# Kernel tuning notes

Measured on AMD Instinct MI355X. Metric: run time of the kernel, lower is better.

Reference implementation:

```python
import jax, jax.numpy as jnp
import numpy as np

RADIUS = 5
ALPHA = 200.0
N, H, W = 8, 352, 352


def _maxpool5(x):
    # F.max_pool2d(kernel=5, stride=1, padding=2); torch pads with -inf for max pool
    return jax.lax.reduce_window(
        x, -jnp.inf, jax.lax.max,
        window_dimensions=(1, 1, 5, 5), window_strides=(1, 1, 1, 1),
        padding=[(0, 0), (0, 0), (2, 2), (2, 2)])


def setup_inputs() -> dict:
    key = jax.random.key(0)
    k1, k2 = jax.random.split(key)
    pred = jax.random.uniform(k1, (N, 1, H, W), dtype=jnp.float32)
    feat = jax.random.uniform(k2, (N, 3, H, W), dtype=jnp.float32)
    return {"pred": pred, "feat": feat}


def reference(pred, feat):
    # interpolate(pred, scale_factor=1.0) and interpolate(feat, size=pred HxW)
    # are identities here (same spatial size, bilinear align_corners).
    sal_map = pred
    image_ = feat

    # contour mask: dilation - erosion of thresholded saliency
    lbl = (sal_map > 0.5).astype(sal_map.dtype)
    ero = 1.0 - _maxpool5(1.0 - lbl)
    dil = _maxpool5(lbl)
    mask = dil - ero  # (N,1,H,W)

    features = jnp.concatenate([image_, sal_map], axis=1)  # (N,4,H,W)
    n, c, h, w = features.shape
    r = RADIUS
    # zero padding matches F.unfold's implicit zero padding
    fpad = jnp.pad(features, ((0, 0), (0, 0), (r, r), (r, r)))
    center_rgb = features[:, :3]   # (N,3,H,W)
    center_sal = features[:, 3:]   # (N,1,H,W)

    # On-the-fly sliding-window reduction instead of materializing the
    # (N,4,11,11,H,W) unfold tensor. 121 static shifts (fixed small set).
    loss_map = jnp.zeros((n, 1, h, w), dtype=features.dtype)
    for dy in range(2 * r + 1):
        for dx in range(2 * r + 1):
            win = fpad[:, :, dy:dy + h, dx:dx + w]  # (N,4,H,W)
            d_rgb = win[:, :3] - center_rgb
            d_sal = jnp.abs(win[:, 3:] - center_sal)
            wgt = jnp.exp(-ALPHA * jnp.sum(d_rgb * d_rgb, axis=1, keepdims=True))
            loss_map = loss_map + wgt * d_sal

    loss = jnp.sum(loss_map * mask) / (jnp.sum(mask) + 1e-6)
    return loss
```

## Files before the change

kernel.cpp:

```cpp
#include <hip/hip_runtime.h>

#define NB 8
#define HH 352
#define WW 352
#define TX 32
#define TY 32
#define TLH 37
#define TLW 42
#define LSTRIDE 43
#define MH 37
#define MW 42
#define MSTRIDE 44
#define TILES_X 11
#define TILES_Y 11
#define NBLK (TILES_X * TILES_Y * NB)

#define RGB_SCALE 16.98644781888824f

typedef float f32x2 __attribute__((ext_vector_type(2)));

__device__ __forceinline__ float elem(float4 q, int c) {
    return c == 0 ? q.x : c == 1 ? q.y : c == 2 ? q.z : q.w;
}

__device__ __forceinline__ void tap_pair(const float4& w, float mq,
                                         f32x2 ncx, f32x2 ncy, f32x2 ncz, f32x2 ncw,
                                         f32x2& accP, f32x2& accQ) {
    f32x2 d0 = ncx + w.x;
    f32x2 d1 = ncy + w.y;
    f32x2 d2 = ncz + w.z;
    f32x2 s  = d0 * d0;
    s += d1 * d1;
    s += d2 * d2;
    f32x2 ds = ncw + w.w;
    f32x2 v;
    v.x = __builtin_amdgcn_exp2f(-s.x) * fabsf(ds.x);
    v.y = __builtin_amdgcn_exp2f(-s.y) * fabsf(ds.y);
    accP += v;
    f32x2 mqv; mqv.x = mq; mqv.y = mq;
    accQ += v * mqv;
}

__device__ __forceinline__ void tap_scalar(const float4& w, float mq,
                                           float ncx, float ncy, float ncz, float ncw,
                                           float& aP, float& aQ) {
    float d0 = w.x + ncx, d1 = w.y + ncy, d2 = w.z + ncz;
    float s = fmaf(d0, d0, fmaf(d1, d1, d2 * d2));
    float v = __builtin_amdgcn_exp2f(-s) * fabsf(w.w + ncw);
    aP += v;
    aQ = fmaf(v, mq, aQ);
}

__global__ __launch_bounds__(256, 2)
void btm_loss_kernel(const float* __restrict__ pred,
                     const float* __restrict__ feat,
                     float2* __restrict__ partials) {
    __shared__ __align__(16) float4 tile[TLH * LSTRIDE];
    __shared__ __align__(16) float  maskp[MH * MSTRIDE];
    __shared__ unsigned long long hbuf[41];
    __shared__ unsigned long long nhbuf[41];
    __shared__ unsigned long long Mbuf[37];
    __shared__ float2 wred[4];

    const int bid = blockIdx.x;
    const int tx_blk = bid % TILES_X;
    const int ty_blk = (bid / TILES_X) % TILES_Y;
    const int n = bid / (TILES_X * TILES_Y);
    const int x0 = tx_blk * TX;
    const int y0 = ty_blk * TY;

    const size_t plane = (size_t)HH * WW;
    const float* fr = feat + ((size_t)n * 3 + 0) * plane;
    const float* fg = feat + ((size_t)n * 3 + 1) * plane;
    const float* fb = feat + ((size_t)n * 3 + 2) * plane;
    const float* ps = pred + (size_t)n * plane;

    const int t = threadIdx.x;

    {
        const int wv = t >> 6, ln = t & 63;
        for (int r = wv; r < 41; r += 4) {
            int gy = y0 + r - 2;
            int gx = x0 - 7 + ln;
            bool inimg = ((unsigned)gy < (unsigned)HH) &&
                         ((unsigned)gx < (unsigned)WW) && (ln < 46);
            float sv = inimg ? ps[gy * WW + gx] : 0.f;
            unsigned long long lb = __ballot(inimg && (sv > 0.5f));
            unsigned long long nb = __ballot(inimg && (sv <= 0.5f));
            unsigned long long a2 = lb | (lb >> 1); a2 |= (a2 >> 2); a2 |= (lb >> 4);
            unsigned long long b2 = nb | (nb >> 1); b2 |= (b2 >> 2); b2 |= (nb >> 4);
            if (ln == 0) { hbuf[r] = a2; nhbuf[r] = b2; }
        }
    }

    for (int i = t; i < TLH * TLW; i += 256) {
        int lr = i / TLW;
        int lc = i - lr * TLW;
        int gy = y0 + lr;
        int gx = x0 + lc - 5;
        float4 v = make_float4(0.f, 0.f, 0.f, 0.f);
        if ((unsigned)gy < (unsigned)HH && (unsigned)gx < (unsigned)WW) {
            int gi = gy * WW + gx;
            v.x = fr[gi] * RGB_SCALE;
            v.y = fg[gi] * RGB_SCALE;
            v.z = fb[gi] * RGB_SCALE;
            v.w = ps[gi];
        }
        tile[lr * LSTRIDE + lc] = v;
    }
    __syncthreads();

    if (t < 37) {
        int lo = 5 - x0; if (lo < 0) lo = 0;
        int hi = WW + 5 - x0; if (hi > 42) hi = 42;
        unsigned long long cm = ((1ull << hi) - 1) & ~((1ull << lo) - 1);
        unsigned long long D = hbuf[t], E = nhbuf[t];
        #pragma unroll
        for (int k = 1; k < 5; ++k) { D |= hbuf[t + k]; E |= nhbuf[t + k]; }
        Mbuf[t] = (y0 + t < HH) ? (D & E & cm) : 0ull;
    }
    __syncthreads();

    for (int i = t; i < MH * MW; i += 256) {
        int mr = i / MW, mc = i - mr * MW;
        maskp[mr * MSTRIDE + mc] = (float)((Mbuf[mr] >> mc) & 1ull);
    }
    __syncthreads();

    const int txq = t & 7;
    const int ty  = t >> 3;
    const int px0 = txq * 4;

    const float4* trow = tile + ty * LSTRIDE + px0;
    const float*  mrow = maskp + ty * MSTRIDE + px0;

    float4 c0 = trow[5], c1 = trow[6], c2 = trow[7], c3 = trow[8];
    f32x2 n01x = {-c0.x, -c1.x}, n01y = {-c0.y, -c1.y}, n01z = {-c0.z, -c1.z}, n01w = {-c0.w, -c1.w};
    f32x2 n23x = {-c2.x, -c3.x}, n23y = {-c2.y, -c3.y}, n23z = {-c2.z, -c3.z}, n23w = {-c2.w, -c3.w};

    f32x2 aP01 = {0.f, 0.f}, aP23 = {0.f, 0.f};
    f32x2 aQ01 = {0.f, 0.f}, aQ23 = {0.f, 0.f};
    float sP0 = 0.f, sP1 = 0.f, sP2 = 0.f, sP3 = 0.f, sQ = 0.f;

    float4 mf0[3];
    #pragma unroll
    for (int q = 0; q < 3; ++q) mf0[q] = *(const float4*)&mrow[4 + 4 * q];
    {
        float4 w0[8];
        #pragma unroll
        for (int j = 0; j < 8; ++j) w0[j] = trow[6 + j];

        tap_scalar(w0[0], elem(mf0[0], 2), n01x.x, n01y.x, n01z.x, n01w.x, sP0, sQ);
        #pragma unroll
        for (int j = 1; j <= 4; ++j)
            tap_pair(w0[j], elem(mf0[(j + 2) >> 2], (j + 2) & 3), n01x, n01y, n01z, n01w, aP01, aQ01);
        tap_scalar(w0[5], elem(mf0[1], 3), n01x.y, n01y.y, n01z.y, n01w.y, sP1, sQ);
        tap_scalar(w0[2], elem(mf0[1], 0), n23x.x, n23y.x, n23z.x, n23w.x, sP2, sQ);
        #pragma unroll
        for (int j = 3; j <= 6; ++j)
            tap_pair(w0[j], elem(mf0[(j + 2) >> 2], (j + 2) & 3), n23x, n23y, n23z, n23w, aP23, aQ23);
        tap_scalar(w0[7], elem(mf0[2], 1), n23x.y, n23y.y, n23z.y, n23w.y, sP3, sQ);
    }

    #pragma unroll 1
    for (int dy = 1; dy <= 5; ++dy) {
        float4 w[14];
        #pragma unroll
        for (int j = 0; j < 14; ++j) w[j] = trow[dy * LSTRIDE + j];
        float4 mf[4];
        const float* mro = mrow + dy * MSTRIDE;
        #pragma unroll
        for (int q = 0; q < 4; ++q) mf[q] = *(const float4*)&mro[4 * q];

        tap_scalar(w[0], elem(mf[0], 0), n01x.x, n01y.x, n01z.x, n01w.x, sP0, sQ);
        #pragma unroll
        for (int j = 1; j <= 10; ++j)
            tap_pair(w[j], elem(mf[j >> 2], j & 3), n01x, n01y, n01z, n01w, aP01, aQ01);
        tap_scalar(w[11], elem(mf[2], 3), n01x.y, n01y.y, n01z.y, n01w.y, sP1, sQ);
        tap_scalar(w[2],  elem(mf[0], 2), n23x.x, n23y.x, n23z.x, n23w.x, sP2, sQ);
        #pragma unroll
        for (int j = 3; j <= 12; ++j)
            tap_pair(w[j], elem(mf[j >> 2], j & 3), n23x, n23y, n23z, n23w, aP23, aQ23);
        tap_scalar(w[13], elem(mf[3], 1), n23x.y, n23y.y, n23z.y, n23w.y, sP3, sQ);
    }

    float m0 = mf0[0].y, m1 = mf0[0].z, m2 = mf0[0].w, m3 = mf0[1].x;
    float e0 = aP01.x + sP0, e1 = aP01.y + sP1;
    float e2 = aP23.x + sP2, e3 = aP23.y + sP3;

    const bool padblk = (ty_blk == 0) || (tx_blk == 0) || (tx_blk == TILES_X - 1);
    if (padblk) {
        const int gy = y0 + ty;
        const int nneg = (5 - gy) > 0 ? (5 - gy) : 0;
        #pragma unroll
        for (int i = 0; i < 4; ++i) {
            const int gx = x0 + px0 + i;
            const int cl = (5 - gx) > 0 ? (5 - gx) : 0;
            const int cr = (gx - 346) > 0 ? (gx - 346) : 0;
            const int np = nneg * 11 + (5 - nneg) * (cl + cr) + cl;
            if (np > 0) {
                float4 ci = (i == 0) ? c0 : (i == 1) ? c1 : (i == 2) ? c2 : c3;
                float s2 = fmaf(ci.x, ci.x, fmaf(ci.y, ci.y, ci.z * ci.z));
                float vp = __builtin_amdgcn_exp2f(-s2) * ci.w * (float)np;
                if (i == 0) e0 += vp; else if (i == 1) e1 += vp;
                else if (i == 2) e2 += vp; else e3 += vp;
            }
        }
    }

    float num = fmaf(m0, e0, fmaf(m1, e1, fmaf(m2, e2, m3 * e3)))
              + ((aQ01.x + aQ01.y) + (aQ23.x + aQ23.y)) + sQ;
    float den = (m0 + m1) + (m2 + m3);

    #pragma unroll
    for (int off = 32; off > 0; off >>= 1) {
        num += __shfl_down(num, off, 64);
        den += __shfl_down(den, off, 64);
    }
    const int wid  = t >> 6;
    const int lane = t & 63;
    if (lane == 0) wred[wid] = make_float2(num, den);
    __syncthreads();
    if (t == 0) {
        float2 a = wred[0];
        #pragma unroll
        for (int w2 = 1; w2 < 4; ++w2) { a.x += wred[w2].x; a.y += wred[w2].y; }
        partials[bid] = a;
    }
}

__global__ __launch_bounds__(256)
void btm_finalize_kernel(const float2* __restrict__ partials,
                         float* __restrict__ out) {
    __shared__ float2 wred[4];
    float num = 0.f, den = 0.f;
    for (int i = threadIdx.x; i < NBLK; i += 256) {
        float2 p = partials[i];
        num += p.x;
        den += p.y;
    }
    #pragma unroll
    for (int off = 32; off > 0; off >>= 1) {
        num += __shfl_down(num, off, 64);
        den += __shfl_down(den, off, 64);
    }
    int wid  = threadIdx.x >> 6;
    int lane = threadIdx.x & 63;
    if (lane == 0) wred[wid] = make_float2(num, den);
    __syncthreads();
    if (threadIdx.x == 0) {
        float2 a = wred[0];
        #pragma unroll
        for (int w = 1; w < 4; ++w) { a.x += wred[w].x; a.y += wred[w].y; }
        out[0] = a.x / (a.y + 1e-6f);
    }
}

extern "C" void kernel_launch(void* const* d_in, const int* in_sizes, int n_in,
                              void* d_out, int out_size, void* d_ws, size_t ws_size,
                              hipStream_t stream) {
    const float* pred = (const float*)d_in[0];
    const float* feat = (const float*)d_in[1];
    float* out = (float*)d_out;
    float2* partials = (float2*)d_ws;

    btm_loss_kernel<<<dim3(NBLK), dim3(256), 0, stream>>>(pred, feat, partials);
    btm_finalize_kernel<<<dim3(1), dim3(256), 0, stream>>>(partials, out);
}
```

Baseline: 95.23 us.

## Use 512-thread blocks with two pixels per thread and XCD-aware block remap

Doubles the block size to 512 threads, so each thread now computes two pixels instead of four. This halves per-thread registers and accumulators, meant to raise occupancy and latency hiding. Blocks are also remapped so that consecutive block IDs (likely dispatched round-robin across XCDs) cover tiles of the same image, aiming for L2 locality. The cost is less reuse of each loaded window value across pixels, which means more LDS reads per tap, plus larger block-wide reductions.

```diff
diff --git a/kernel.cpp b/kernel.cpp
--- a/kernel.cpp
+++ b/kernel.cpp
@@ -18,10 +18,6 @@
 #define RGB_SCALE 16.98644781888824f
 
 typedef float f32x2 __attribute__((ext_vector_type(2)));
-
-__device__ __forceinline__ float elem(float4 q, int c) {
-    return c == 0 ? q.x : c == 1 ? q.y : c == 2 ? q.z : q.w;
-}
 
 __device__ __forceinline__ void tap_pair(const float4& w, float mq,
                                          f32x2 ncx, f32x2 ncy, f32x2 ncz, f32x2 ncw,
@@ -51,7 +47,7 @@
     aQ = fmaf(v, mq, aQ);
 }
 
-__global__ __launch_bounds__(256, 2)
+__global__ __launch_bounds__(512)
 void btm_loss_kernel(const float* __restrict__ pred,
                      const float* __restrict__ feat,
                      float2* __restrict__ partials) {
@@ -60,9 +56,10 @@
     __shared__ unsigned long long hbuf[41];
     __shared__ unsigned long long nhbuf[41];
     __shared__ unsigned long long Mbuf[37];
-    __shared__ float2 wred[4];
-
-    const int bid = blockIdx.x;
+    __shared__ float2 wred[8];
+
+    const int braw = blockIdx.x;
+    const int bid  = (braw & 7) * (TILES_X * TILES_Y) + (braw >> 3);
     const int tx_blk = bid % TILES_X;
     const int ty_blk = (bid / TILES_X) % TILES_Y;
     const int n = bid / (TILES_X * TILES_Y);
@@ -79,7 +76,7 @@
 
     {
         const int wv = t >> 6, ln = t & 63;
-        for (int r = wv; r < 41; r += 4) {
+        for (int r = wv; r < 41; r += 8) {
             int gy = y0 + r - 2;
             int gx = x0 - 7 + ln;
             bool inimg = ((unsigned)gy < (unsigned)HH) &&
@@ -93,7 +90,7 @@
         }
     }
 
-    for (int i = t; i < TLH * TLW; i += 256) {
+    for (int i = t; i < TLH * TLW; i += 512) {
         int lr = i / TLW;
         int lc = i - lr * TLW;
         int gy = y0 + lr;
@@ -121,96 +118,88 @@
     }
     __syncthreads();
 
-    for (int i = t; i < MH * MW; i += 256) {
+    for (int i = t; i < MH * MW; i += 512) {
         int mr = i / MW, mc = i - mr * MW;
         maskp[mr * MSTRIDE + mc] = (float)((Mbuf[mr] >> mc) & 1ull);
     }
     __syncthreads();
 
-    const int txq = t & 7;
-    const int ty  = t >> 3;
-    const int px0 = txq * 4;
+    const int txq = t & 15;
+    const int ty  = t >> 4;
+    const int px0 = txq * 2;
 
     const float4* trow = tile + ty * LSTRIDE + px0;
     const float*  mrow = maskp + ty * MSTRIDE + px0;
 
-    float4 c0 = trow[5], c1 = trow[6], c2 = trow[7], c3 = trow[8];
-    f32x2 n01x = {-c0.x, -c1.x}, n01y = {-c0.y, -c1.y}, n01z = {-c0.z, -c1.z}, n01w = {-c0.w, -c1.w};
-    f32x2 n23x = {-c2.x, -c3.x}, n23y = {-c2.y, -c3.y}, n23z = {-c2.z, -c3.z}, n23w = {-c2.w, -c3.w};
-
-    f32x2 aP01 = {0.f, 0.f}, aP23 = {0.f, 0.f};
-    f32x2 aQ01 = {0.f, 0.f}, aQ23 = {0.f, 0.f};
-    float sP0 = 0.f, sP1 = 0.f, sP2 = 0.f, sP3 = 0.f, sQ = 0.f;
-
-    float4 mf0[3];
-    #pragma unroll
-    for (int q = 0; q < 3; ++q) mf0[q] = *(const float4*)&mrow[4 + 4 * q];
+    float4 c0 = trow[5], c1 = trow[6];
+    f32x2 ncx = {-c0.x, -c1.x}, ncy = {-c0.y, -c1.y},
+          ncz = {-c0.z, -c1.z}, ncw = {-c0.w, -c1.w};
+
+    f32x2 aP = {0.f, 0.f}, aQ = {0.f, 0.f};
+    float sP0 = 0.f, sP1 = 0.f, sQ = 0.f;
+    float m0, m1;
+
     {
-        float4 w0[8];
-        #pragma unroll
-        for (int j = 0; j < 8; ++j) w0[j] = trow[6 + j];
-
-        tap_scalar(w0[0], elem(mf0[0], 2), n01x.x, n01y.x, n01z.x, n01w.x, sP0, sQ);
-        #pragma unroll
-        for (int j = 1; j <= 4; ++j)
-            tap_pair(w0[j], elem(mf0[(j + 2) >> 2], (j + 2) & 3), n01x, n01y, n01z, n01w, aP01, aQ01);
-        tap_scalar(w0[5], elem(mf0[1], 3), n01x.y, n01y.y, n01z.y, n01w.y, sP1, sQ);
-        tap_scalar(w0[2], elem(mf0[1], 0), n23x.x, n23y.x, n23z.x, n23w.x, sP2, sQ);
-        #pragma unroll
-        for (int j = 3; j <= 6; ++j)
-            tap_pair(w0[j], elem(mf0[(j + 2) >> 2], (j + 2) & 3), n23x, n23y, n23z, n23w, aP23, aQ23);
-        tap_scalar(w0[7], elem(mf0[2], 1), n23x.y, n23y.y, n23z.y, n23w.y, sP3, sQ);
+        float2 ma = *(const float2*)&mrow[4];
+        float2 mb = *(const float2*)&mrow[6];
+        float2 mc2 = *(const float2*)&mrow[8];
+        float2 md = *(const float2*)&mrow[10];
+        m0 = ma.y;
+        m1 = mb.x;
+
+        float4 w6 = trow[6], w7 = trow[7], w8 = trow[8], w9 = trow[9],
+               w10 = trow[10], w11 = trow[11];
+        tap_scalar(w6,  mb.x, ncx.x, ncy.x, ncz.x, ncw.x, sP0, sQ);
+        tap_pair(w7,  mb.y,  ncx, ncy, ncz, ncw, aP, aQ);
+        tap_pair(w8,  mc2.x, ncx, ncy, ncz, ncw, aP, aQ);
+        tap_pair(w9,  mc2.y, ncx, ncy, ncz, ncw, aP, aQ);
+        tap_pair(w10, md.x,  ncx, ncy, ncz, ncw, aP, aQ);
+        tap_scalar(w11, md.y, ncx.y, ncy.y, ncz.y, ncw.y, sP1, sQ);
     }
 
     #pragma unroll 1
     for (int dy = 1; dy <= 5; ++dy) {
-        float4 w[14];
-        #pragma unroll
-        for (int j = 0; j < 14; ++j) w[j] = trow[dy * LSTRIDE + j];
-        float4 mf[4];
-        const float* mro = mrow + dy * MSTRIDE;
-        #pragma unroll
-        for (int q = 0; q < 4; ++q) mf[q] = *(const float4*)&mro[4 * q];
-
-        tap_scalar(w[0], elem(mf[0], 0), n01x.x, n01y.x, n01z.x, n01w.x, sP0, sQ);
-        #pragma unroll
-        for (int j = 1; j <= 10; ++j)
-            tap_pair(w[j], elem(mf[j >> 2], j & 3), n01x, n01y, n01z, n01w, aP01, aQ01);
-        tap_scalar(w[11], elem(mf[2], 3), n01x.y, n01y.y, n01z.y, n01w.y, sP1, sQ);
-        tap_scalar(w[2],  elem(mf[0], 2), n23x.x, n23y.x, n23z.x, n23w.x, sP2, sQ);
-        #pragma unroll
-        for (int j = 3; j <= 12; ++j)
-            tap_pair(w[j], elem(mf[j >> 2], j & 3), n23x, n23y, n23z, n23w, aP23, aQ23);
-        tap_scalar(w[13], elem(mf[3], 1), n23x.y, n23y.y, n23z.y, n23w.y, sP3, sQ);
-    }
-
-    float m0 = mf0[0].y, m1 = mf0[0].z, m2 = mf0[0].w, m3 = mf0[1].x;
-    float e0 = aP01.x + sP0, e1 = aP01.y + sP1;
-    float e2 = aP23.x + sP2, e3 = aP23.y + sP3;
+        const float4* wr = trow + dy * LSTRIDE;
+        const float*  mr = mrow + dy * MSTRIDE;
+        float4 w[12];
+        #pragma unroll
+        for (int j = 0; j < 12; ++j) w[j] = wr[j];
+        float2 mp[6];
+        #pragma unroll
+        for (int q = 0; q < 6; ++q) mp[q] = *(const float2*)&mr[2 * q];
+
+        tap_scalar(w[0], mp[0].x, ncx.x, ncy.x, ncz.x, ncw.x, sP0, sQ);
+        #pragma unroll
+        for (int j = 1; j <= 10; ++j) {
+            float mq = (j & 1) ? mp[j >> 1].y : mp[j >> 1].x;
+            tap_pair(w[j], mq, ncx, ncy, ncz, ncw, aP, aQ);
+        }
+        tap_scalar(w[11], mp[5].y, ncx.y, ncy.y, ncz.y, ncw.y, sP1, sQ);
+    }
+
+    float e0 = aP.x + sP0, e1 = aP.y + sP1;
 
     const bool padblk = (ty_blk == 0) || (tx_blk == 0) || (tx_blk == TILES_X - 1);
     if (padblk) {
         const int gy = y0 + ty;
         const int nneg = (5 - gy) > 0 ? (5 - gy) : 0;
         #pragma unroll
-        for (int i = 0; i < 4; ++i) {
+        for (int i = 0; i < 2; ++i) {
             const int gx = x0 + px0 + i;
             const int cl = (5 - gx) > 0 ? (5 - gx) : 0;
             const int cr = (gx - 346) > 0 ? (gx - 346) : 0;
             const int np = nneg * 11 + (5 - nneg) * (cl + cr) + cl;
             if (np > 0) {
-                float4 ci = (i == 0) ? c0 : (i == 1) ? c1 : (i == 2) ? c2 : c3;
+                float4 ci = (i == 0) ? c0 : c1;
                 float s2 = fmaf(ci.x, ci.x, fmaf(ci.y, ci.y, ci.z * ci.z));
                 float vp = __builtin_amdgcn_exp2f(-s2) * ci.w * (float)np;
-                if (i == 0) e0 += vp; else if (i == 1) e1 += vp;
-                else if (i == 2) e2 += vp; else e3 += vp;
+                if (i == 0) e0 += vp; else e1 += vp;
             }
         }
     }
 
-    float num = fmaf(m0, e0, fmaf(m1, e1, fmaf(m2, e2, m3 * e3)))
-              + ((aQ01.x + aQ01.y) + (aQ23.x + aQ23.y)) + sQ;
-    float den = (m0 + m1) + (m2 + m3);
+    float num = fmaf(m0, e0, m1 * e1) + (aQ.x + aQ.y) + sQ;
+    float den = m0 + m1;
 
     #pragma unroll
     for (int off = 32; off > 0; off >>= 1) {
@@ -224,7 +213,7 @@
     if (t == 0) {
         float2 a = wred[0];
         #pragma unroll
-        for (int w2 = 1; w2 < 4; ++w2) { a.x += wred[w2].x; a.y += wred[w2].y; }
+        for (int w2 = 1; w2 < 8; ++w2) { a.x += wred[w2].x; a.y += wred[w2].y; }
         partials[bid] = a;
     }
 }
@@ -264,6 +253,6 @@
     float* out = (float*)d_out;
     float2* partials = (float2*)d_ws;
 
-    btm_loss_kernel<<<dim3(NBLK), dim3(256), 0, stream>>>(pred, feat, partials);
+    btm_loss_kernel<<<dim3(NBLK), dim3(512), 0, stream>>>(pred, feat, partials);
     btm_finalize_kernel<<<dim3(1), dim3(256), 0, stream>>>(partials, out);
 }
```

After: 90.04 us. 5.5% less time.
